# Kernel tuning notes

Measured on AMD Instinct MI355X. Metric: run time of the kernel, lower is better.

## Reference

```python
import jax, jax.numpy as jnp
import numpy as np

DIM = 192
NUM_HEADS = 6
WIN = (4, 4, 4)
SHIFT = (2, 2, 2)


def setup_inputs() -> dict:
    key = jax.random.key(0)
    k_x, k_qw, k_qb, k_pw, k_pb = jax.random.split(key, 5)
    C = DIM
    x = jax.random.normal(k_x, (1, C, 64, 64, 64), dtype=jnp.float32)
    lim = 1.0 / np.sqrt(C)
    qkv_w = jax.random.uniform(k_qw, (3 * C, C), minval=-lim, maxval=lim, dtype=jnp.float32)
    qkv_b = jax.random.uniform(k_qb, (3 * C,), minval=-lim, maxval=lim, dtype=jnp.float32)
    proj_w = jax.random.uniform(k_pw, (C, C), minval=-lim, maxval=lim, dtype=jnp.float32)
    proj_b = jax.random.uniform(k_pb, (C,), minval=-lim, maxval=lim, dtype=jnp.float32)
    return {"x": x, "qkv_w": qkv_w, "qkv_b": qkv_b, "proj_w": proj_w, "proj_b": proj_b}


def reference(x, qkv_w, qkv_b, proj_w, proj_b):
    B, C, X, Y, Z = x.shape
    Wx, Wy, Wz = WIN
    Sx, Sy, Sz = SHIFT
    H = NUM_HEADS
    hd = C // H
    scale = hd ** -0.5
    # cyclic shift
    x = jnp.roll(x, shift=(-Sx, -Sy, -Sz), axis=(2, 3, 4))
    nWx, nWy, nWz = X // Wx, Y // Wy, Z // Wz
    # window partition: (B,C,X,Y,Z) -> (B*nW, N_tok, C)
    h = x.reshape(B, C, nWx, Wx, nWy, Wy, nWz, Wz)
    h = jnp.transpose(h, (0, 2, 4, 6, 3, 5, 7, 1))  # (B,nWx,nWy,nWz,Wx,Wy,Wz,C)
    N_tok = Wx * Wy * Wz
    nW = B * nWx * nWy * nWz
    h = h.reshape(nW, N_tok, C)
    # qkv projection
    qkv = h @ qkv_w.T + qkv_b  # (nW, N, 3C)
    qkv = qkv.reshape(nW, N_tok, 3, H, hd)
    qkv = jnp.transpose(qkv, (2, 0, 3, 1, 4))  # (3, nW, H, N, hd)
    q, k, v = qkv[0], qkv[1], qkv[2]
    # scaled dot-product attention within each window
    attn = jnp.einsum('whqd,whkd->whqk', q, k) * scale
    attn = jax.nn.softmax(attn, axis=-1)
    out = jnp.einsum('whqk,whkd->whqd', attn, v)  # (nW, H, N, hd)
    out = jnp.transpose(out, (0, 2, 1, 3)).reshape(nW, N_tok, C)
    out = out @ proj_w.T + proj_b
    # window reverse: (nW, N, C) -> (B, C, X, Y, Z)
    out = out.reshape(B, nWx, nWy, nWz, Wx, Wy, Wz, C)
    out = jnp.transpose(out, (0, 7, 1, 4, 2, 5, 3, 6))
    out = out.reshape(B, C, X, Y, Z)
    out = jnp.roll(out, shift=(Sx, Sy, Sz), axis=(2, 3, 4))
    return out
```

## Files before the change

### kernel.cpp

```cpp
#include <hip/hip_runtime.h>
#include <stdint.h>

#define V_ELEMS (64*64*64)

typedef _Float16 f16x8 __attribute__((ext_vector_type(8)));
typedef _Float16 f16x4 __attribute__((ext_vector_type(4)));
typedef float f32x4 __attribute__((ext_vector_type(4)));

#define SMEM_BYTES 53248
#define H_STRIDE 200
#define QKP_STRIDE 72
#define VT_STRIDE 72
#define OH_STRIDE 72

#define W16_BYTES  294912
#define HWS_BYTES  100663296
#define OWS_BYTES  201326592

__global__ void cvt_weights_kernel(const float* __restrict__ qkv_w,
                                   const float* __restrict__ proj_w,
                                   _Float16* __restrict__ w16) {
    int i = blockIdx.x * 256 + threadIdx.x;
    if (i < 110592)      w16[i] = (_Float16)qkv_w[i];
    else if (i < 147456) w16[i] = (_Float16)proj_w[i - 110592];
}

__global__ __launch_bounds__(256, 6)
void gather_kernel(const float* __restrict__ x, _Float16* __restrict__ hws) {
    __shared__ _Float16 L[64 * 200];
    const int xg = blockIdx.x >> 6, yg = blockIdx.x & 63;
    const int tid = threadIdx.x;

    {
        const int zq = tid & 15, cb = tid >> 4;
#pragma unroll
        for (int u = 0; u < 12; ++u) {
            const int c = cb + 16 * u;
            const float4 v = *(const float4*)(x + ((size_t)c * 4096 + (size_t)xg * 64 + yg) * 64 + zq * 4);
            const int z0 = zq * 4;
            L[(z0 + 0) * 200 + c] = (_Float16)v.x;
            L[(z0 + 1) * 200 + c] = (_Float16)v.y;
            L[(z0 + 2) * 200 + c] = (_Float16)v.z;
            L[(z0 + 3) * 200 + c] = (_Float16)v.w;
        }
    }
    __syncthreads();

    const int tx = (xg + 62) & 63, wx = tx >> 2, i = tx & 3;
    const int ty = (yg + 62) & 63, wy = ty >> 2, j = ty & 3;
    const int rowbase = i * 16 + j * 4;
#pragma unroll
    for (int u = 0; u < 6; ++u) {
        const int t   = u * 256 + tid;
        const int wz  = t / 96;
        const int rem = t % 96;
        const int zl  = rem / 24;
        const int ch  = rem % 24;
        const int zg  = (wz * 4 + 2 + zl) & 63;
        const size_t dst = (size_t)((wx * 16 + wy) * 16 + wz) * 12288
                         + (size_t)(rowbase + zl) * 192 + ch * 8;
        *(f16x8*)(hws + dst) = *(const f16x8*)(L + zg * 200 + ch * 8);
    }
}

__global__ __launch_bounds__(256, 3)
void scatter_kernel(const float* __restrict__ ows, const float* __restrict__ proj_b,
                    float* __restrict__ out) {
    __shared__ float L[64 * 193];
    const int xg = blockIdx.x >> 6, yg = blockIdx.x & 63;
    const int tid = threadIdx.x;

    const int tx = (xg + 62) & 63, wx = tx >> 2, i = tx & 3;
    const int ty = (yg + 62) & 63, wy = ty >> 2, j = ty & 3;
    const int Wbase = (wx * 16 + wy) * 16;
    const int rowbase = i * 16 + j * 4;

#pragma unroll
    for (int u = 0; u < 12; ++u) {
        const int f  = tid + 256 * u;
        const int wz = f / 192;
        const int q  = f % 192;
        const int zl = q / 48;
        const int c4 = q % 48;
        const float4 v = *(const float4*)(ows
            + (size_t)(Wbase + wz) * 12288 + (size_t)(rowbase + zl) * 192 + c4 * 4);
        const int a = wz * 4 + zl;
        float* Lp = L + a * 193 + c4 * 4;
        Lp[0] = v.x; Lp[1] = v.y; Lp[2] = v.z; Lp[3] = v.w;
    }
    __syncthreads();

    const int zq = tid & 15;
    const int cb = tid >> 4;
#pragma unroll
    for (int u = 0; u < 12; ++u) {
        const int c = cb + 16 * u;
        const float bias = proj_b[c];
        float4 v;
        float* vp = (float*)&v;
#pragma unroll
        for (int k = 0; k < 4; ++k) {
            const int a = (zq * 4 + k + 62) & 63;
            vp[k] = L[a * 193 + c] + bias;
        }
        *(float4*)(out + ((size_t)c * 4096 + (size_t)xg * 64 + yg) * 64 + zq * 4) = v;
    }
}

template<int GWS, int SWS>
__global__ __launch_bounds__(256, 3)
void win_attn_kernel(const float* __restrict__ x,
                     const _Float16* __restrict__ w16,
                     const float* __restrict__ qkv_b,
                     const float* __restrict__ proj_b,
                     float* __restrict__ out,
                     const _Float16* __restrict__ hws,
                     float* __restrict__ ows)
{
    extern __shared__ char smem[];
    _Float16* h_s  = (_Float16*)smem;
    _Float16* qk_s = (_Float16*)(smem + 25600);
    _Float16* P_s  = (_Float16*)(smem + 25600);
    _Float16* vt_s = (_Float16*)(smem + 44032);
    _Float16* oh_s = (_Float16*)(smem + 44032);

    const _Float16* qw16 = w16;
    const _Float16* pw16 = w16 + 110592;

    const int tid  = threadIdx.x;
    const int wave = tid >> 6;
    const int lane = tid & 63;
    const int l15  = lane & 15;
    const int quad = lane >> 4;

    const int hh = (wave >> 1) & 1;
    const int dh = wave & 1;

    const int bid = blockIdx.x;
    const int xcd = bid & 7;
    const int s_  = bid >> 3;
    const int wzl = s_ & 3;
    const int gi  = (s_ >> 2) * 8 + xcd;
    const int wx  = gi >> 6;
    const int wy  = (gi >> 2) & 15;
    const int wz  = ((gi & 3) << 2) | wzl;
    const int W   = (wx * 16 + wy) * 16 + wz;

    if (GWS) {
        const size_t wbase = (size_t)W * 12288;
        const int row = tid >> 2, part = tid & 3;
#pragma unroll
        for (int u = 0; u < 6; ++u) {
            const int c8 = part + 4 * u;
            f16x8 v = *(const f16x8*)(hws + wbase + (size_t)row * 192 + c8 * 8);
            *(f16x8*)(h_s + row * H_STRIDE + c8 * 8) = v;
        }
    } else {
        const int p  = tid & 1;
        const int r  = (tid >> 1) & 15;
        const int cb = tid >> 5;
        const int i = r >> 2, j = r & 3;
        const int xg = (wx*4 + i + 2) & 63;
        const int yg = (wy*4 + j + 2) & 63;
        const int zg = (wz*4 + 2 + 2*p) & 63;
        const int tok = r*4 + 2*p;
        const size_t sbase = ((size_t)xg*64 + (size_t)yg)*64 + (size_t)zg;
#pragma unroll
        for (int t = 0; t < 24; ++t) {
            int c = cb + 8*t;
            float2 v = *(const float2*)(x + (size_t)c*V_ELEMS + sbase);
            h_s[tok*H_STRIDE + c]     = (_Float16)v.x;
            h_s[(tok+1)*H_STRIDE + c] = (_Float16)v.y;
        }
    }

    f32x4 out_acc[3][4];
#pragma unroll
    for (int a = 0; a < 3; ++a)
#pragma unroll
        for (int b = 0; b < 4; ++b)
            out_acc[a][b] = (f32x4){0.f, 0.f, 0.f, 0.f};

    const f32x4 fzero = {0.f, 0.f, 0.f, 0.f};
    __syncthreads();

#pragma unroll
    for (int hp = 0; hp < 3; ++hp) {
        f16x8 bfr[3][6];
        float wbias[3];
#pragma unroll
        for (int wh = 0; wh < 3; ++wh) {
            const int n = wh*192 + (2*hp + hh)*32 + dh*16 + l15;
            wbias[wh] = qkv_b[n];
#pragma unroll
            for (int ks = 0; ks < 6; ++ks)
                bfr[wh][ks] = *(const f16x8*)(qw16 + (size_t)n*192 + ks*32 + quad*8);
        }
        __builtin_amdgcn_s_setprio(1);
#pragma unroll
        for (int rt = 0; rt < 4; ++rt) {
            f16x8 af[6];
#pragma unroll
            for (int ks = 0; ks < 6; ++ks)
                af[ks] = *(const f16x8*)(h_s + (rt*16 + l15)*H_STRIDE + ks*32 + quad*8);
#pragma unroll
            for (int wh = 0; wh < 3; ++wh) {
                f32x4 acc = fzero;
#pragma unroll
                for (int ks = 0; ks < 6; ++ks)
                    acc = __builtin_amdgcn_mfma_f32_16x16x32_f16(af[ks], bfr[wh][ks], acc, 0, 0, 0);
                if (wh == 2) {
                    f16x4 pk;
#pragma unroll
                    for (int r2 = 0; r2 < 4; ++r2) pk[r2] = (_Float16)(acc[r2] + wbias[2]);
                    *(f16x4*)(vt_s + (hh*32 + dh*16 + l15)*VT_STRIDE + rt*16 + quad*4) = pk;
                } else {
                    _Float16* dst = qk_s + hh*64*QKP_STRIDE + (wh == 1 ? 32 : 0);
#pragma unroll
                    for (int r2 = 0; r2 < 4; ++r2)
                        dst[(rt*16 + quad*4 + r2)*QKP_STRIDE + dh*16 + l15] =
                            (_Float16)(acc[r2] + wbias[wh]);
                }
            }
        }
        __builtin_amdgcn_s_setprio(0);
        __syncthreads();

        f32x4 pfr[2][4];
        float inv_r[2][4];
#pragma unroll
        for (int jj = 0; jj < 2; ++jj) {
            f16x8 aq = *(const f16x8*)(qk_s + (jj*64 + wave*16 + l15)*QKP_STRIDE + quad*8);
            f32x4 s[4];
#pragma unroll
            for (int ct = 0; ct < 4; ++ct) {
                f16x8 bk = *(const f16x8*)(qk_s + (jj*64 + ct*16 + l15)*QKP_STRIDE + 32 + quad*8);
                s[ct] = __builtin_amdgcn_mfma_f32_16x16x32_f16(aq, bk, fzero, 0, 0, 0);
            }
            float mx[4];
#pragma unroll
            for (int r = 0; r < 4; ++r) {
                float m = fmaxf(fmaxf(s[0][r], s[1][r]), fmaxf(s[2][r], s[3][r]));
#pragma unroll
                for (int msk = 1; msk < 16; msk <<= 1) m = fmaxf(m, __shfl_xor(m, msk));
                mx[r] = m;
            }
            const float kscale = 0.17677669529663687f * 1.4426950408889634f;
#pragma unroll
            for (int ct = 0; ct < 4; ++ct)
#pragma unroll
                for (int r = 0; r < 4; ++r)
                    s[ct][r] = exp2f((s[ct][r] - mx[r]) * kscale);
#pragma unroll
            for (int r = 0; r < 4; ++r) {
                float sum = s[0][r] + s[1][r] + s[2][r] + s[3][r];
#pragma unroll
                for (int msk = 1; msk < 16; msk <<= 1) sum += __shfl_xor(sum, msk);
                inv_r[jj][r] = 1.0f / sum;
            }
#pragma unroll
            for (int ct = 0; ct < 4; ++ct) pfr[jj][ct] = s[ct];
        }
        __syncthreads();

#pragma unroll
        for (int jj = 0; jj < 2; ++jj)
#pragma unroll
            for (int ct = 0; ct < 4; ++ct)
#pragma unroll
                for (int r = 0; r < 4; ++r)
                    P_s[(jj*64 + wave*16 + quad*4 + r)*QKP_STRIDE + ct*16 + l15] =
                        (_Float16)pfr[jj][ct][r];

        f32x4 oacc[2][2];
#pragma unroll
        for (int jj = 0; jj < 2; ++jj)
#pragma unroll
            for (int ct = 0; ct < 2; ++ct) oacc[jj][ct] = fzero;
#pragma unroll
        for (int jj = 0; jj < 2; ++jj)
#pragma unroll
            for (int ks = 0; ks < 2; ++ks) {
                f16x8 ap = *(const f16x8*)(P_s + (jj*64 + wave*16 + l15)*QKP_STRIDE + ks*32 + quad*8);
#pragma unroll
                for (int ct = 0; ct < 2; ++ct) {
                    f16x8 bv = *(const f16x8*)(vt_s + (jj*32 + ct*16 + l15)*VT_STRIDE + ks*32 + quad*8);
                    oacc[jj][ct] = __builtin_amdgcn_mfma_f32_16x16x32_f16(ap, bv, oacc[jj][ct], 0, 0, 0);
                }
            }
        __syncthreads();

#pragma unroll
        for (int jj = 0; jj < 2; ++jj)
#pragma unroll
            for (int ct = 0; ct < 2; ++ct)
#pragma unroll
                for (int r = 0; r < 4; ++r)
                    oh_s[(wave*16 + quad*4 + r)*OH_STRIDE + jj*32 + ct*16 + l15] =
                        (_Float16)(oacc[jj][ct][r] * inv_r[jj][r]);
        __syncthreads();

        f16x8 afr[4][2];
#pragma unroll
        for (int rt = 0; rt < 4; ++rt)
#pragma unroll
            for (int ks = 0; ks < 2; ++ks)
                afr[rt][ks] = *(const f16x8*)(oh_s + (rt*16 + l15)*OH_STRIDE + ks*32 + quad*8);
        __builtin_amdgcn_s_setprio(1);
#pragma unroll
        for (int cti = 0; cti < 3; ++cti) {
            const int n = (wave + 4*cti)*16 + l15;
#pragma unroll
            for (int ks = 0; ks < 2; ++ks) {
                f16x8 bf = *(const f16x8*)(pw16 + (size_t)n*192 + hp*64 + ks*32 + quad*8);
#pragma unroll
                for (int rt = 0; rt < 4; ++rt)
                    out_acc[cti][rt] =
                        __builtin_amdgcn_mfma_f32_16x16x32_f16(afr[rt][ks], bf, out_acc[cti][rt], 0, 0, 0);
            }
        }
        __builtin_amdgcn_s_setprio(0);
        __syncthreads();
    }

    if (SWS) {
        const size_t obase = (size_t)W * 12288;
#pragma unroll
        for (int cti = 0; cti < 3; ++cti) {
            const int n = (wave + 4*cti)*16 + l15;
#pragma unroll
            for (int rt = 0; rt < 4; ++rt)
#pragma unroll
                for (int r = 0; r < 4; ++r)
                    ows[obase + (size_t)(rt*16 + quad*4 + r)*192 + n] = out_acc[cti][rt][r];
        }
    } else {
        const int zA = wz*4 + 2;
        const int zB = (wz*4 + 4) & 63;
        const int yg = (wy*4 + quad + 2) & 63;
#pragma unroll
        for (int cti = 0; cti < 3; ++cti) {
            const int n = (wave + 4*cti)*16 + l15;
            const float bias = proj_b[n];
#pragma unroll
            for (int rt = 0; rt < 4; ++rt) {
                const int xg = (wx*4 + rt + 2) & 63;
                const size_t base = (((size_t)n*64 + (size_t)xg)*64 + (size_t)yg)*64;
                float2 v01 = { out_acc[cti][rt][0] + bias, out_acc[cti][rt][1] + bias };
                float2 v23 = { out_acc[cti][rt][2] + bias, out_acc[cti][rt][3] + bias };
                *(float2*)(out + base + zA) = v01;
                *(float2*)(out + base + zB) = v23;
            }
        }
    }
}

extern "C" void kernel_launch(void* const* d_in, const int* in_sizes, int n_in,
                              void* d_out, int out_size, void* d_ws, size_t ws_size,
                              hipStream_t stream) {
    const float* x      = (const float*)d_in[0];
    const float* qkv_w  = (const float*)d_in[1];
    const float* qkv_b  = (const float*)d_in[2];
    const float* proj_w = (const float*)d_in[3];
    const float* proj_b = (const float*)d_in[4];
    float* out = (float*)d_out;
    char* wsb = (char*)d_ws;
    _Float16* w16 = (_Float16*)wsb;

    cvt_weights_kernel<<<dim3(576), dim3(256), 0, stream>>>(qkv_w, proj_w, w16);

    if (ws_size >= (size_t)W16_BYTES + HWS_BYTES + OWS_BYTES) {
        _Float16* hws = (_Float16*)(wsb + W16_BYTES);
        float*    ows = (float*)(wsb + W16_BYTES + HWS_BYTES);
        gather_kernel<<<dim3(4096), dim3(256), 0, stream>>>(x, hws);
        win_attn_kernel<1,1><<<dim3(4096), dim3(256), SMEM_BYTES, stream>>>(
            x, w16, qkv_b, proj_b, out, hws, ows);
        scatter_kernel<<<dim3(4096), dim3(256), 0, stream>>>(ows, proj_b, out);
    } else if (ws_size >= (size_t)W16_BYTES + OWS_BYTES) {
        float* ows = (float*)(wsb + W16_BYTES);
        win_attn_kernel<0,1><<<dim3(4096), dim3(256), SMEM_BYTES, stream>>>(
            x, w16, qkv_b, proj_b, out, (const _Float16*)nullptr, ows);
        scatter_kernel<<<dim3(4096), dim3(256), 0, stream>>>(ows, proj_b, out);
    } else {
        win_attn_kernel<0,0><<<dim3(4096), dim3(256), SMEM_BYTES, stream>>>(
            x, w16, qkv_b, proj_b, out, (const _Float16*)nullptr, (float*)nullptr);
    }
}
```

Baseline: 624.5 us.

## XOR-swizzle shared memory tiles and stage workspace output through LDS

Applies an XOR swizzle on 16-byte chunks to every shared-memory tile (h, q/k, P, V^T, per-head output) so that MFMA fragment loads and scattered stores spread across LDS banks instead of conflicting. The workspace-output path now transposes accumulators through a padded LDS buffer in two halves and writes coalesced float4 rows instead of scattered scalar stores. This adds index arithmetic and extra barriers in exchange for fewer bank conflicts and better global write coalescing.

```diff
diff --git a/kernel.cpp b/kernel.cpp
--- a/kernel.cpp
+++ b/kernel.cpp
@@ -132,6 +132,7 @@
     const int lane = tid & 63;
     const int l15  = lane & 15;
     const int quad = lane >> 4;
+    const int sw   = l15 & 7;
 
     const int hh = (wave >> 1) & 1;
     const int dh = wave & 1;
@@ -153,7 +154,7 @@
         for (int u = 0; u < 6; ++u) {
             const int c8 = part + 4 * u;
             f16x8 v = *(const f16x8*)(hws + wbase + (size_t)row * 192 + c8 * 8);
-            *(f16x8*)(h_s + row * H_STRIDE + c8 * 8) = v;
+            *(f16x8*)(h_s + row * H_STRIDE + (c8 ^ (row & 7)) * 8) = v;
         }
     } else {
         const int p  = tid & 1;
@@ -169,8 +170,8 @@
         for (int t = 0; t < 24; ++t) {
             int c = cb + 8*t;
             float2 v = *(const float2*)(x + (size_t)c*V_ELEMS + sbase);
-            h_s[tok*H_STRIDE + c]     = (_Float16)v.x;
-            h_s[(tok+1)*H_STRIDE + c] = (_Float16)v.y;
+            h_s[tok*H_STRIDE + (((c>>3) ^ (tok&7))<<3) + (c&7)]         = (_Float16)v.x;
+            h_s[(tok+1)*H_STRIDE + (((c>>3) ^ ((tok+1)&7))<<3) + (c&7)] = (_Float16)v.y;
         }
     }
 
@@ -202,7 +203,7 @@
             f16x8 af[6];
 #pragma unroll
             for (int ks = 0; ks < 6; ++ks)
-                af[ks] = *(const f16x8*)(h_s + (rt*16 + l15)*H_STRIDE + ks*32 + quad*8);
+                af[ks] = *(const f16x8*)(h_s + (rt*16 + l15)*H_STRIDE + ((ks*4 + quad) ^ sw)*8);
 #pragma unroll
             for (int wh = 0; wh < 3; ++wh) {
                 f32x4 acc = fzero;
@@ -213,13 +214,17 @@
                     f16x4 pk;
 #pragma unroll
                     for (int r2 = 0; r2 < 4; ++r2) pk[r2] = (_Float16)(acc[r2] + wbias[2]);
-                    *(f16x4*)(vt_s + (hh*32 + dh*16 + l15)*VT_STRIDE + rt*16 + quad*4) = pk;
+                    *(f16x4*)(vt_s + (hh*32 + dh*16 + l15)*VT_STRIDE
+                              + (((rt*2 + (quad>>1)) ^ sw)<<3) + (quad&1)*4) = pk;
                 } else {
-                    _Float16* dst = qk_s + hh*64*QKP_STRIDE + (wh == 1 ? 32 : 0);
-#pragma unroll
-                    for (int r2 = 0; r2 < 4; ++r2)
-                        dst[(rt*16 + quad*4 + r2)*QKP_STRIDE + dh*16 + l15] =
+                    _Float16* dst = qk_s + hh*64*QKP_STRIDE;
+                    const int ck = (wh == 1 ? 4 : 0) + dh*2 + (l15>>3);
+#pragma unroll
+                    for (int r2 = 0; r2 < 4; ++r2) {
+                        const int row = rt*16 + quad*4 + r2;
+                        dst[row*QKP_STRIDE + ((ck ^ (row&7))<<3) + (l15&7)] =
                             (_Float16)(acc[r2] + wbias[wh]);
+                    }
                 }
             }
         }
@@ -230,11 +235,11 @@
         float inv_r[2][4];
 #pragma unroll
         for (int jj = 0; jj < 2; ++jj) {
-            f16x8 aq = *(const f16x8*)(qk_s + (jj*64 + wave*16 + l15)*QKP_STRIDE + quad*8);
+            f16x8 aq = *(const f16x8*)(qk_s + (jj*64 + wave*16 + l15)*QKP_STRIDE + (quad ^ sw)*8);
             f32x4 s[4];
 #pragma unroll
             for (int ct = 0; ct < 4; ++ct) {
-                f16x8 bk = *(const f16x8*)(qk_s + (jj*64 + ct*16 + l15)*QKP_STRIDE + 32 + quad*8);
+                f16x8 bk = *(const f16x8*)(qk_s + (jj*64 + ct*16 + l15)*QKP_STRIDE + ((4 + quad) ^ sw)*8);
                 s[ct] = __builtin_amdgcn_mfma_f32_16x16x32_f16(aq, bk, fzero, 0, 0, 0);
             }
             float mx[4];
@@ -268,9 +273,12 @@
 #pragma unroll
             for (int ct = 0; ct < 4; ++ct)
 #pragma unroll
-                for (int r = 0; r < 4; ++r)
-                    P_s[(jj*64 + wave*16 + quad*4 + r)*QKP_STRIDE + ct*16 + l15] =
+                for (int r = 0; r < 4; ++r) {
+                    const int rsw = (quad*4 + r) & 7;
+                    P_s[(jj*64 + wave*16 + quad*4 + r)*QKP_STRIDE
+                        + (((ct*2 + (l15>>3)) ^ rsw)<<3) + (l15&7)] =
                         (_Float16)pfr[jj][ct][r];
+                }
 
         f32x4 oacc[2][2];
 #pragma unroll
@@ -281,10 +289,10 @@
         for (int jj = 0; jj < 2; ++jj)
 #pragma unroll
             for (int ks = 0; ks < 2; ++ks) {
-                f16x8 ap = *(const f16x8*)(P_s + (jj*64 + wave*16 + l15)*QKP_STRIDE + ks*32 + quad*8);
+                f16x8 ap = *(const f16x8*)(P_s + (jj*64 + wave*16 + l15)*QKP_STRIDE + ((ks*4 + quad) ^ sw)*8);
 #pragma unroll
                 for (int ct = 0; ct < 2; ++ct) {
-                    f16x8 bv = *(const f16x8*)(vt_s + (jj*32 + ct*16 + l15)*VT_STRIDE + ks*32 + quad*8);
+                    f16x8 bv = *(const f16x8*)(vt_s + (jj*32 + ct*16 + l15)*VT_STRIDE + ((ks*4 + quad) ^ sw)*8);
                     oacc[jj][ct] = __builtin_amdgcn_mfma_f32_16x16x32_f16(ap, bv, oacc[jj][ct], 0, 0, 0);
                 }
             }
@@ -295,9 +303,12 @@
 #pragma unroll
             for (int ct = 0; ct < 2; ++ct)
 #pragma unroll
-                for (int r = 0; r < 4; ++r)
-                    oh_s[(wave*16 + quad*4 + r)*OH_STRIDE + jj*32 + ct*16 + l15] =
+                for (int r = 0; r < 4; ++r) {
+                    const int rsw = (quad*4 + r) & 7;
+                    oh_s[(wave*16 + quad*4 + r)*OH_STRIDE
+                         + (((jj*4 + ct*2 + (l15>>3)) ^ rsw)<<3) + (l15&7)] =
                         (_Float16)(oacc[jj][ct][r] * inv_r[jj][r]);
+                }
         __syncthreads();
 
         f16x8 afr[4][2];
@@ -305,7 +316,7 @@
         for (int rt = 0; rt < 4; ++rt)
 #pragma unroll
             for (int ks = 0; ks < 2; ++ks)
-                afr[rt][ks] = *(const f16x8*)(oh_s + (rt*16 + l15)*OH_STRIDE + ks*32 + quad*8);
+                afr[rt][ks] = *(const f16x8*)(oh_s + (rt*16 + l15)*OH_STRIDE + ((ks*4 + quad) ^ sw)*8);
         __builtin_amdgcn_s_setprio(1);
 #pragma unroll
         for (int cti = 0; cti < 3; ++cti) {
@@ -324,15 +335,34 @@
     }
 
     if (SWS) {
+        float* st = (float*)smem;
         const size_t obase = (size_t)W * 12288;
 #pragma unroll
-        for (int cti = 0; cti < 3; ++cti) {
-            const int n = (wave + 4*cti)*16 + l15;
-#pragma unroll
-            for (int rt = 0; rt < 4; ++rt)
-#pragma unroll
-                for (int r = 0; r < 4; ++r)
-                    ows[obase + (size_t)(rt*16 + quad*4 + r)*192 + n] = out_acc[cti][rt][r];
+        for (int p = 0; p < 2; ++p) {
+            __syncthreads();
+#pragma unroll
+            for (int cti = 0; cti < 3; ++cti) {
+                const int nb = wave + 4*cti;
+                if (nb >= p*6 && nb < p*6 + 6) {
+                    const int cl = nb*16 - p*96 + l15;
+#pragma unroll
+                    for (int rt = 0; rt < 4; ++rt)
+#pragma unroll
+                        for (int r = 0; r < 4; ++r)
+                            st[(rt*16 + quad*4 + r)*97 + cl] = out_acc[cti][rt][r];
+                }
+            }
+            __syncthreads();
+#pragma unroll
+            for (int u = 0; u < 6; ++u) {
+                const int t = u*256 + tid;
+                const int row = t / 24, c4 = t % 24;
+                float4 v;
+                float* vp = (float*)&v;
+#pragma unroll
+                for (int k = 0; k < 4; ++k) vp[k] = st[row*97 + c4*4 + k];
+                *(float4*)(ows + obase + (size_t)row*192 + p*96 + c4*4) = v;
+            }
         }
     } else {
         const int zA = wz*4 + 2;
```

New measurement: 818.3 us. 1.31x slower.
